# Kernel tuning notes

Hardware: AMD Instinct MI355X
Metric: run time of the kernel (lower is better)

Reference implementation:

```python
import jax, jax.numpy as jnp
import numpy as np

EPS = 1e-05
FACT = 2.0
REJECT_RATIO = 1.0


def setup_inputs() -> dict:
    key = jax.random.key(0)
    k1, k2 = jax.random.split(key)
    B, N = 8, 4096
    pc1 = jax.random.normal(k1, (B, 4, N), dtype=jnp.float32)
    pc2 = jax.random.normal(k2, (B, 4, N), dtype=jnp.float32)
    # homogeneous coordinates: last row = 1
    pc1 = pc1.at[:, 3, :].set(1.0)
    pc2 = pc2.at[:, 3, :].set(1.0)
    return {"pc1": pc1, "pc2": pc2}


def _rot_to_quat(R):
    # standard rotation-matrix -> quaternion (w, x, y, z)
    r00, r11, r22 = R[0, 0], R[1, 1], R[2, 2]
    qw = 0.5 * jnp.sqrt(jnp.maximum(1e-12, 1.0 + r00 + r11 + r22))
    qx = 0.5 * jnp.sqrt(jnp.maximum(0.0, 1.0 + r00 - r11 - r22))
    qy = 0.5 * jnp.sqrt(jnp.maximum(0.0, 1.0 - r00 + r11 - r22))
    qz = 0.5 * jnp.sqrt(jnp.maximum(0.0, 1.0 - r00 - r11 + r22))
    qx = jnp.where(R[2, 1] - R[1, 2] < 0, -qx, qx)
    qy = jnp.where(R[0, 2] - R[2, 0] < 0, -qy, qy)
    qz = jnp.where(R[1, 0] - R[0, 1] < 0, -qz, qz)
    return jnp.stack([qw, qx, qy, qz])


def _normalize_rotmat(R):
    # operates on COLUMNS, like the torch code (R[:, 2] etc.)
    z = R[:, 2] / jnp.linalg.norm(R[:, 2])
    y = R[:, 1]
    x = jnp.cross(y, z)
    x = x / jnp.linalg.norm(x)
    y = jnp.cross(z, x)
    return jnp.stack([x, y, z], axis=1)


def _norm_tf(pc):
    # T = diag(1/std) @ [I | -mean]  (std is unbiased, as torch.std)
    std = jnp.std(pc[:3, :], axis=1, ddof=1)
    mean = jnp.mean(pc[:3, :], axis=1)
    T = jnp.zeros((4, 4), dtype=pc.dtype)
    T = T.at[jnp.arange(3), jnp.arange(3)].set(1.0 / std)
    T = T.at[:3, 3].set(-mean / std)
    T = T.at[3, 3].set(1.0)
    return T


def _per_sample(pc1, pc2):
    # ---- soft_knn: pairwise squared distance over xyz ----
    p1, p2 = pc1[:3], pc2[:3]  # (3, N)
    d = ((p1 ** 2).sum(0)[:, None]
         - 2.0 * jnp.einsum('dn,dm->nm', p1, p2)
         + (p2 ** 2).sum(0)[None, :])            # (N1, N2)
    W = jax.nn.softmax(FACT / jnp.clip(d, EPS, None), axis=1)
    pc_nearest = pc2 @ W.T                        # (4, N1) soft-gathered points

    # ---- soft_outlier_rejection ----
    dist = jnp.linalg.norm(pc1 - pc_nearest, axis=0)
    filt = jax.nn.sigmoid((dist - dist.mean() * REJECT_RATIO - EPS) * -1e10)

    # ---- dlt(pc1, pc_nearest, filt) ----
    T2 = _norm_tf(pc_nearest)
    pc2n = T2 @ pc_nearest
    T1 = _norm_tf(pc1)
    pc1n = T1 @ pc1

    mask = (filt > 0.5).astype(pc1.dtype)         # hard inlier mask (sigmoid slope 1e10)
    N = pc1.shape[1]
    a = pc1n.T                                    # (N, 4)
    z4 = jnp.zeros((N, 4), dtype=pc1.dtype)
    row0 = jnp.concatenate([z4, -pc2n[2][:, None] * a, pc2n[1][:, None] * a], axis=1)
    row1 = jnp.concatenate([pc2n[2][:, None] * a, z4, -pc2n[0][:, None] * a], axis=1)
    M = (jnp.stack([row0, row1], axis=1) * mask[:, None, None]).reshape(2 * N, 12)

    _, _, Vh = jnp.linalg.svd(M, full_matrices=False)
    p = Vh[-1]                                    # null-space vector (12,)
    p = jnp.where(p[10] < 0, -p, p)
    p = p / jnp.sqrt(p[8] ** 2 + p[9] ** 2 + p[10] ** 2)

    T = jnp.zeros((4, 4), dtype=pc1.dtype)
    T = T.at[:3, :].set(p.reshape(3, 4)).at[3, 3].set(1.0)
    T = jnp.linalg.inv(T2) @ T @ T1
    R = _normalize_rotmat(T[:3, :3])
    T = T.at[:3, :3].set(R)
    return T, _rot_to_quat(R), T[:3, 3]


def reference(pc1, pc2):
    T, q, t = jax.vmap(_per_sample)(pc1, pc2)
    return T, q, t
```

## Files before the change

### kernel.cpp

```cpp
#include <hip/hip_runtime.h>
#include <math.h>

#define NPTS 4096
#define EPSC 1e-5f
#define F2C (2.0f*1.44269504088896340736f)

#if __has_builtin(__builtin_amdgcn_exp2f)
#define FEXP2 __builtin_amdgcn_exp2f
#else
#define FEXP2(x) __expf((x)*0.6931471805599453f)
#endif

#define IDX(i,j) ((i)*((i)+1)/2 + (j))

template<int CHN>
__global__ void __launch_bounds__(256) k_soft(const float* __restrict__ pc1,
                                              const float* __restrict__ pc2,
                                              float* __restrict__ part){
  constexpr int NC = NPTS/CHN;
  int bid = blockIdx.x;
  int chunk = bid & (NC-1), rb = (bid/NC) & 15, b = bid/(NC*16);

  __shared__ float4 sp[CHN];
  {
    const float* p2 = pc2 + (size_t)b*4*NPTS + chunk*CHN;
    for (int m = threadIdx.x; m < CHN; m += 256){
      float x = p2[m], y = p2[m+NPTS], z = p2[m+2*NPTS];
      sp[m] = make_float4(x, y, z, x*x + y*y + z*z);
    }
  }
  __syncthreads();

  int n = rb*256 + threadIdx.x;
  const float* p1 = pc1 + (size_t)b*4*NPTS + n;
  float x1 = p1[0], y1 = p1[NPTS], z1 = p1[2*NPTS];
  float q1 = x1*x1 + y1*y1 + z1*z1;
  float mx = -2.f*x1, my = -2.f*y1, mz = -2.f*z1;

  float4 c0 = sp[0];
  float d0 = fmaf(mx,c0.x, fmaf(my,c0.y, fmaf(mz,c0.z, c0.w + q1)));
  float m_ = F2C * __builtin_amdgcn_rcpf(fmaxf(d0, EPSC));
  float L = 1.f, Ax = c0.x, Ay = c0.y, Az = c0.z;

  #pragma unroll 8
  for (int mm=1; mm<CHN; ++mm){
    float4 c = sp[mm];
    float d = fmaf(mx,c.x, fmaf(my,c.y, fmaf(mz,c.z, c.w + q1)));
    float dinv = __builtin_amdgcn_rcpf(fmaxf(d, EPSC));
    float t = fmaf(F2C, dinv, -m_);
    if (__any(t > 0.f)){
      float tp = fmaxf(t, 0.f);
      float sc = FEXP2(-tp);
      L *= sc; Ax *= sc; Ay *= sc; Az *= sc;
      m_ += tp;
      t = fminf(t, 0.f);
    }
    float pe = FEXP2(t);
    L += pe;
    Ax = fmaf(pe,c.x,Ax); Ay = fmaf(pe,c.y,Ay); Az = fmaf(pe,c.z,Az);
  }
  float* pp = part + ((size_t)(b*NC + chunk)*5)*NPTS + n;
  pp[0]=m_; pp[NPTS]=L; pp[2*NPTS]=Ax; pp[3*NPTS]=Ay; pp[4*NPTS]=Az;
}

template<int NC>
__global__ void __launch_bounds__(512) k_merge(const float* __restrict__ pc1,
                                               const float* __restrict__ part,
                                               float* __restrict__ pcn,
                                               float* __restrict__ dist,
                                               float* __restrict__ psum13){
  int b = blockIdx.x >> 4, rb = blockIdx.x & 15;
  int t = threadIdx.x & 255, half = threadIdx.x >> 8;
  int n = rb*256 + t;
  constexpr int H = NC/2;
  float sc[H], Lc[H], Axc[H], Ayc[H], Azc[H];
  float S = -3.4e38f;
  #pragma unroll
  for (int c=0;c<H;c++){
    const float* pp = part + ((size_t)(b*NC + half*H + c)*5)*NPTS + n;
    sc[c]=pp[0]; Lc[c]=pp[NPTS]; Axc[c]=pp[2*NPTS]; Ayc[c]=pp[3*NPTS]; Azc[c]=pp[4*NPTS];
    S = fmaxf(S, sc[c]);
  }
  float L=0.f, Ax=0.f, Ay=0.f, Az=0.f;
  #pragma unroll
  for (int c=0;c<H;c++){
    float w = FEXP2(sc[c]-S);
    L=fmaf(w,Lc[c],L); Ax=fmaf(w,Axc[c],Ax); Ay=fmaf(w,Ayc[c],Ay); Az=fmaf(w,Azc[c],Az);
  }
  __shared__ float ex[256][5];
  if (half==1){ ex[t][0]=S; ex[t][1]=L; ex[t][2]=Ax; ex[t][3]=Ay; ex[t][4]=Az; }
  __syncthreads();
  __shared__ float red[4][13];
  if (half==0){
    float S1=ex[t][0];
    float M = fmaxf(S,S1);
    float w0=FEXP2(S-M), w1=FEXP2(S1-M);
    L = w0*L + w1*ex[t][1];
    Ax = w0*Ax + w1*ex[t][2];
    Ay = w0*Ay + w1*ex[t][3];
    Az = w0*Az + w1*ex[t][4];
    float inv = 1.f/L;
    float px=Ax*inv, py=Ay*inv, pz=Az*inv;
    const float* p1 = pc1 + (size_t)b*4*NPTS + n;
    float x1=p1[0], y1=p1[NPTS], z1=p1[2*NPTS];
    float dx=x1-px, dy=y1-py, dz=z1-pz;
    float dd=sqrtf(dx*dx+dy*dy+dz*dz);
    pcn[(size_t)(b*3+0)*NPTS+n]=px;
    pcn[(size_t)(b*3+1)*NPTS+n]=py;
    pcn[(size_t)(b*3+2)*NPTS+n]=pz;
    dist[(size_t)b*NPTS+n]=dd;
    float acc[13]={x1,y1,z1,x1*x1,y1*y1,z1*z1,px,py,pz,px*px,py*py,pz*pz,dd};
    int lane = t & 63, wv = t >> 6;
    #pragma unroll
    for (int k=0;k<13;k++){
      float v = acc[k];
      v += __shfl_xor(v,32); v += __shfl_xor(v,16); v += __shfl_xor(v,8);
      v += __shfl_xor(v,4);  v += __shfl_xor(v,2);  v += __shfl_xor(v,1);
      if (lane==0) red[wv][k]=v;
    }
  }
  __syncthreads();
  if (threadIdx.x<13)
    psum13[(size_t)blockIdx.x*13 + threadIdx.x] =
      red[0][threadIdx.x]+red[1][threadIdx.x]+red[2][threadIdx.x]+red[3][threadIdx.x];
}

__device__ __forceinline__ float elemA(const float* S, int i, int k){
  int bi=i>>2, bj=k>>2;
  int ii=i&3, jj=k&3;
  int lo = ii<jj?ii:jj, hi = ii<jj?jj:ii;
  int pe = 4*lo - ((lo*(lo-1))>>1) + (hi-lo);
  int w;
  if (bi==bj) w = (bi==2)?30:0;
  else {
    int blo = bi<bj?bi:bj, bhi = bi<bj?bj:bi;
    if (blo==0 && bhi==1) return 0.f;
    w = (blo==0)?10:20;
  }
  return S[w+pe];
}

__global__ void __launch_bounds__(256) k_solve(const float* __restrict__ pc1,
                                               const float* __restrict__ pcn,
                                               const float* __restrict__ dist,
                                               const float* __restrict__ psum13,
                                               float* __restrict__ out){
  int b=blockIdx.x, t=threadIdx.x;
  __shared__ float stot[13];
  __shared__ float sst[13];
  if (t<13){
    float s=0.f;
    #pragma unroll
    for (int i=0;i<16;i++) s += psum13[(size_t)(b*16+i)*13 + t];
    stot[t]=s;
  }
  __syncthreads();
  if (t==0){
    const float Nf = 4096.f, Nm1 = 4095.f;
    #pragma unroll
    for (int j=0;j<3;j++){
      float m  = stot[j]/Nf;
      float v  = (stot[3+j]-Nf*m*m)/Nm1;
      sst[j]=m; sst[3+j]=sqrtf(fmaxf(v,0.f));
      float m2 = stot[6+j]/Nf;
      float v2 = (stot[9+j]-Nf*m2*m2)/Nm1;
      sst[6+j]=m2; sst[9+j]=sqrtf(fmaxf(v2,0.f));
    }
    sst[12]=stot[12]/Nf;
  }
  __syncthreads();
  float i1x=1.f/sst[3], i1y=1.f/sst[4], i1z=1.f/sst[5];
  float t1x=-sst[0]/sst[3], t1y=-sst[1]/sst[4], t1z=-sst[2]/sst[5];
  float i2x=1.f/sst[9], i2y=1.f/sst[10], i2z=1.f/sst[11];
  float t2x=-sst[6]/sst[9], t2y=-sst[7]/sst[10], t2z=-sst[8]/sst[11];
  float meanD=sst[12];

  float acc[40];
  #pragma unroll
  for (int k=0;k<40;k++) acc[k]=0.f;
  #pragma unroll 4
  for (int i=0;i<16;i++){
    int n=i*256+t;
    const float* p1 = pc1 + (size_t)b*4*NPTS + n;
    float X1=fmaf(p1[0],i1x,t1x), Y1=fmaf(p1[NPTS],i1y,t1y), Z1=fmaf(p1[2*NPTS],i1z,t1z);
    float X2=fmaf(pcn[(size_t)(b*3+0)*NPTS+n],i2x,t2x);
    float Y2=fmaf(pcn[(size_t)(b*3+1)*NPTS+n],i2y,t2y);
    float Z2=fmaf(pcn[(size_t)(b*3+2)*NPTS+n],i2z,t2z);
    float zthr = (dist[(size_t)b*NPTS+n] - meanD) - EPSC;
    float msk = (zthr < 0.f) ? 1.f : 0.f;
    float tz = msk*Z2;
    float wA = tz*Z2, wB = -tz*X2, wC = -tz*Y2;
    float wD = msk*fmaf(X2,X2,Y2*Y2);
    float ee[10]={X1*X1, X1*Y1, X1*Z1, X1, Y1*Y1, Y1*Z1, Y1, Z1*Z1, Z1, 1.f};
    #pragma unroll
    for (int j=0;j<10;j++){
      acc[j]    = fmaf(wA,ee[j],acc[j]);
      acc[10+j] = fmaf(wB,ee[j],acc[10+j]);
      acc[20+j] = fmaf(wC,ee[j],acc[20+j]);
      acc[30+j] = fmaf(wD,ee[j],acc[30+j]);
    }
  }
  __shared__ float red[4][40];
  __shared__ float SS[40];
  {
    int lane=t&63, wv=t>>6;
    #pragma unroll
    for (int k=0;k<40;k++){
      float v=acc[k];
      v+=__shfl_xor(v,32); v+=__shfl_xor(v,16); v+=__shfl_xor(v,8);
      v+=__shfl_xor(v,4);  v+=__shfl_xor(v,2);  v+=__shfl_xor(v,1);
      if(lane==0) red[wv][k]=v;
    }
  }
  __syncthreads();
  if (t<40) SS[t]=red[0][t]+red[1][t]+red[2][t]+red[3][t];
  __syncthreads();

  if (t<64){
    float a[78];
    #pragma unroll
    for (int i=0;i<12;i++)
      #pragma unroll
      for (int j=0;j<=i;j++)
        a[IDX(i,j)] = elemA(SS,i,j);
    {
      float tr=0.f;
      #pragma unroll
      for (int i=0;i<12;i++) tr += a[IDX(i,i)];
      float eps = 1e-5f * tr * (1.f/12.f);
      #pragma unroll
      for (int i=0;i<12;i++) a[IDX(i,i)] += eps;
    }
    #pragma unroll
    for (int j=0;j<12;j++){
      float s = a[IDX(j,j)];
      #pragma unroll
      for (int k=0;k<j;k++) s = fmaf(-a[IDX(j,k)], a[IDX(j,k)], s);
      float d = sqrtf(fmaxf(s, 1e-30f));
      a[IDX(j,j)] = d;
      float dinv = __builtin_amdgcn_rcpf(d);
      #pragma unroll
      for (int i=j+1;i<12;i++){
        float s2 = a[IDX(i,j)];
        #pragma unroll
        for (int k=0;k<j;k++) s2 = fmaf(-a[IDX(i,k)], a[IDX(j,k)], s2);
        a[IDX(i,j)] = s2 * dinv;
      }
    }
    float y[12], Brow[12];
    #pragma unroll
    for (int i=0;i<12;i++){
      float s = (i==t) ? 1.f : 0.f;
      #pragma unroll
      for (int k=0;k<i;k++) s = fmaf(-a[IDX(i,k)], y[k], s);
      y[i] = s * __builtin_amdgcn_rcpf(a[IDX(i,i)]);
    }
    #pragma unroll
    for (int i=11;i>=0;i--){
      float s = y[i];
      #pragma unroll
      for (int k=11;k>i;k--) s = fmaf(-a[IDX(k,i)], Brow[k], s);
      Brow[i] = s * __builtin_amdgcn_rcpf(a[IDX(i,i)]);
    }
    {
      float mxv = 0.f;
      #pragma unroll
      for (int i=0;i<12;i++) mxv = fmaxf(mxv, fabsf(Brow[i]));
      mxv = fmaxf(mxv, __shfl_xor(mxv,1)); mxv = fmaxf(mxv, __shfl_xor(mxv,2));
      mxv = fmaxf(mxv, __shfl_xor(mxv,4)); mxv = fmaxf(mxv, __shfl_xor(mxv,8));
      float sc = __builtin_amdgcn_rcpf(mxv);
      #pragma unroll
      for (int i=0;i<12;i++) Brow[i] *= sc;
    }
    #pragma unroll
    for (int rep=0; rep<2; ++rep){
      float nr[12];
      #pragma unroll
      for (int i=0;i<12;i++) nr[i]=0.f;
      #pragma unroll
      for (int k=0;k<12;k++){
        float bjk = Brow[k];
        #pragma unroll
        for (int m2=0;m2<12;m2++){
          float bkm = __shfl(Brow[m2], k);
          nr[m2] = fmaf(bjk, bkm, nr[m2]);
        }
      }
      float mxv = 0.f;
      #pragma unroll
      for (int i=0;i<12;i++) mxv = fmaxf(mxv, fabsf(nr[i]));
      mxv = fmaxf(mxv, __shfl_xor(mxv,1)); mxv = fmaxf(mxv, __shfl_xor(mxv,2));
      mxv = fmaxf(mxv, __shfl_xor(mxv,4)); mxv = fmaxf(mxv, __shfl_xor(mxv,8));
      float sc = __builtin_amdgcn_rcpf(mxv);
      #pragma unroll
      for (int i=0;i<12;i++) Brow[i] = nr[i]*sc;
    }
    float v = 0.f;
    #pragma unroll
    for (int i=0;i<12;i++) v += Brow[i];
    #pragma unroll
    for (int it=0; it<14; ++it){
      float w = 0.f;
      #pragma unroll
      for (int k=0;k<12;k++) w = fmaf(Brow[k], __shfl(v,k), w);
      float nn = w*w;
      nn += __shfl_xor(nn,1); nn += __shfl_xor(nn,2);
      nn += __shfl_xor(nn,4); nn += __shfl_xor(nn,8);
      v = w * rsqrtf(nn);
    }
    float pvf[12];
    #pragma unroll
    for (int i=0;i<12;i++) pvf[i] = __shfl(v, i);

    if (t==0){
      double pv[12];
      #pragma unroll
      for (int i=0;i<12;i++) pv[i]=(double)pvf[i];
      if (pv[10]<0.0){
        #pragma unroll
        for (int i=0;i<12;i++) pv[i]=-pv[i];
      }
      double nrm = sqrt(pv[8]*pv[8]+pv[9]*pv[9]+pv[10]*pv[10]);
      #pragma unroll
      for (int i=0;i<12;i++) pv[i]/=nrm;
      double m1[3]={sst[0],sst[1],sst[2]}, sd1[3]={sst[3],sst[4],sst[5]};
      double m2[3]={sst[6],sst[7],sst[8]}, sd2[3]={sst[9],sst[10],sst[11]};
      double Td[3][4]={{pv[0],pv[1],pv[2],pv[3]},
                       {pv[4],pv[5],pv[6],pv[7]},
                       {pv[8],pv[9],pv[10],pv[11]}};
      double F[3][4];
      for (int i=0;i<3;i++){
        double b3 = Td[i][3];
        for (int j=0;j<3;j++){
          F[i][j] = sd2[i]*(Td[i][j]/sd1[j]);
          b3 += Td[i][j]*(-m1[j]/sd1[j]);
        }
        F[i][3] = sd2[i]*b3 + m2[i];
      }
      double zx=F[0][2],zy=F[1][2],zz2=F[2][2];
      double zn=sqrt(zx*zx+zy*zy+zz2*zz2);
      zx/=zn; zy/=zn; zz2/=zn;
      double yx=F[0][1],yy=F[1][1],yz=F[2][1];
      double xx=yy*zz2-yz*zy, xy=yz*zx-yx*zz2, xz=yx*zy-yy*zx;
      double xn=sqrt(xx*xx+xy*xy+xz*xz);
      xx/=xn; xy/=xn; xz/=xn;
      double y2x=zy*xz-zz2*xy, y2y=zz2*xx-zx*xz, y2z=zx*xy-zy*xx;
      double R00=xx,R01=y2x,R02=zx;
      double R10=xy,R11=y2y,R12=zy;
      double R20=xz,R21=y2z,R22=zz2;
      float* oT = out + b*16;
      oT[0]=(float)R00; oT[1]=(float)R01; oT[2]=(float)R02; oT[3]=(float)F[0][3];
      oT[4]=(float)R10; oT[5]=(float)R11; oT[6]=(float)R12; oT[7]=(float)F[1][3];
      oT[8]=(float)R20; oT[9]=(float)R21; oT[10]=(float)R22; oT[11]=(float)F[2][3];
      oT[12]=0.f; oT[13]=0.f; oT[14]=0.f; oT[15]=1.f;
      double qw=0.5*sqrt(fmax(1e-12, 1.0+R00+R11+R22));
      double qx=0.5*sqrt(fmax(0.0, 1.0+R00-R11-R22));
      double qy=0.5*sqrt(fmax(0.0, 1.0-R00+R11-R22));
      double qz=0.5*sqrt(fmax(0.0, 1.0-R00-R11+R22));
      if (R21-R12<0.0) qx=-qx;
      if (R02-R20<0.0) qy=-qy;
      if (R10-R01<0.0) qz=-qz;
      float* oQ = out + 128 + b*4;
      oQ[0]=(float)qw; oQ[1]=(float)qx; oQ[2]=(float)qy; oQ[3]=(float)qz;
      float* ot3 = out + 160 + b*3;
      ot3[0]=(float)F[0][3]; ot3[1]=(float)F[1][3]; ot3[2]=(float)F[2][3];
    }
  }
}

extern "C" void kernel_launch(void* const* d_in, const int* in_sizes, int n_in,
                              void* d_out, int out_size, void* d_ws, size_t ws_size,
                              hipStream_t stream) {
  const float* pc1 = (const float*)d_in[0];
  const float* pc2 = (const float*)d_in[1];
  float* out  = (float*)d_out;
  float* ws   = (float*)d_ws;

  const size_t fixed = 98304 + 32768 + 128*13;
  size_t need16 = ((size_t)8*16*5*NPTS + fixed) * 4;
  int NC = (ws_size >= need16) ? 16 : 8;

  float* part  = ws;
  float* pcn   = part + (size_t)8*NC*5*NPTS;
  float* dist  = pcn + 98304;
  float* psum13= dist + 32768;

  if (NC == 16){
    hipLaunchKernelGGL(k_soft<256>,  dim3(2048), dim3(256), 0, stream, pc1, pc2, part);
    hipLaunchKernelGGL(k_merge<16>,  dim3(128),  dim3(512), 0, stream, pc1, part, pcn, dist, psum13);
  } else {
    hipLaunchKernelGGL(k_soft<512>,  dim3(1024), dim3(256), 0, stream, pc1, pc2, part);
    hipLaunchKernelGGL(k_merge<8>,   dim3(128),  dim3(512), 0, stream, pc1, part, pcn, dist, psum13);
  }
  hipLaunchKernelGGL(k_solve, dim3(8), dim3(256), 0, stream, pc1, pcn, dist, psum13, out);
}
```

Baseline: 156.9 us.

## Skip negligible softmax terms via min-distance prepass and split solve kernel

The soft-kNN kernel now does a first pass to find the minimum distance per query, fixing the softmax max up front. In a second pass it skips whole groups of four candidates when every lane's weight would be below exp2(-100), which removes the online rescaling and most of the exp and reciprocal work. The 40-term moment accumulation moves out of the single-block-per-batch solve into a separate 64-block kernel, leaving a small finalize kernel for the solve. The chunk count is fixed at 8 rather than chosen from workspace size. The cost is an extra distance pass, one more kernel launch, and dropping terms that are numerically negligible.

```diff
diff --git a/kernel.cpp b/kernel.cpp
--- a/kernel.cpp
+++ b/kernel.cpp
@@ -4,6 +4,7 @@
 #define NPTS 4096
 #define EPSC 1e-5f
 #define F2C (2.0f*1.44269504088896340736f)
+#define SKIP_MARGIN 100.0f
 
 #if __has_builtin(__builtin_amdgcn_exp2f)
 #define FEXP2 __builtin_amdgcn_exp2f
@@ -37,27 +38,34 @@
   float q1 = x1*x1 + y1*y1 + z1*z1;
   float mx = -2.f*x1, my = -2.f*y1, mz = -2.f*z1;
 
-  float4 c0 = sp[0];
-  float d0 = fmaf(mx,c0.x, fmaf(my,c0.y, fmaf(mz,c0.z, c0.w + q1)));
-  float m_ = F2C * __builtin_amdgcn_rcpf(fmaxf(d0, EPSC));
-  float L = 1.f, Ax = c0.x, Ay = c0.y, Az = c0.z;
-
+  float dmin = 3.4e38f;
   #pragma unroll 8
-  for (int mm=1; mm<CHN; ++mm){
-    float4 c = sp[mm];
+  for (int m=0; m<CHN; ++m){
+    float4 c = sp[m];
     float d = fmaf(mx,c.x, fmaf(my,c.y, fmaf(mz,c.z, c.w + q1)));
-    float dinv = __builtin_amdgcn_rcpf(fmaxf(d, EPSC));
-    float t = fmaf(F2C, dinv, -m_);
-    if (__any(t > 0.f)){
-      float tp = fmaxf(t, 0.f);
-      float sc = FEXP2(-tp);
-      L *= sc; Ax *= sc; Ay *= sc; Az *= sc;
-      m_ += tp;
-      t = fminf(t, 0.f);
-    }
-    float pe = FEXP2(t);
-    L += pe;
-    Ax = fmaf(pe,c.x,Ax); Ay = fmaf(pe,c.y,Ay); Az = fmaf(pe,c.z,Az);
+    dmin = fminf(dmin, d);
+  }
+  float m_ = F2C * __builtin_amdgcn_rcpf(fmaxf(dmin, EPSC));
+  float r  = m_ - SKIP_MARGIN;
+  float d_thr = (r > 0.f) ? F2C * __builtin_amdgcn_rcpf(r) : 3.4e38f;
+
+  float L=0.f, Ax=0.f, Ay=0.f, Az=0.f;
+  for (int g=0; g<CHN; g+=4){
+    float4 c0=sp[g], c1=sp[g+1], c2=sp[g+2], c3=sp[g+3];
+    float d0 = fmaf(mx,c0.x, fmaf(my,c0.y, fmaf(mz,c0.z, c0.w + q1)));
+    float d1 = fmaf(mx,c1.x, fmaf(my,c1.y, fmaf(mz,c1.z, c1.w + q1)));
+    float d2 = fmaf(mx,c2.x, fmaf(my,c2.y, fmaf(mz,c2.z, c2.w + q1)));
+    float d3 = fmaf(mx,c3.x, fmaf(my,c3.y, fmaf(mz,c3.z, c3.w + q1)));
+    float gmin = fminf(fminf(d0,d1), fminf(d2,d3));
+    if (__all(gmin > d_thr)) continue;
+    float p0 = FEXP2(fmaf(F2C, __builtin_amdgcn_rcpf(fmaxf(d0,EPSC)), -m_));
+    float p1e= FEXP2(fmaf(F2C, __builtin_amdgcn_rcpf(fmaxf(d1,EPSC)), -m_));
+    float p2e= FEXP2(fmaf(F2C, __builtin_amdgcn_rcpf(fmaxf(d2,EPSC)), -m_));
+    float p3e= FEXP2(fmaf(F2C, __builtin_amdgcn_rcpf(fmaxf(d3,EPSC)), -m_));
+    L += (p0+p1e)+(p2e+p3e);
+    Ax = fmaf(p0,c0.x, fmaf(p1e,c1.x, fmaf(p2e,c2.x, fmaf(p3e,c3.x, Ax))));
+    Ay = fmaf(p0,c0.y, fmaf(p1e,c1.y, fmaf(p2e,c2.y, fmaf(p3e,c3.y, Ay))));
+    Az = fmaf(p0,c0.z, fmaf(p1e,c1.z, fmaf(p2e,c2.z, fmaf(p3e,c3.z, Az))));
   }
   float* pp = part + ((size_t)(b*NC + chunk)*5)*NPTS + n;
   pp[0]=m_; pp[NPTS]=L; pp[2*NPTS]=Ax; pp[3*NPTS]=Ay; pp[4*NPTS]=Az;
@@ -125,6 +133,83 @@
       red[0][threadIdx.x]+red[1][threadIdx.x]+red[2][threadIdx.x]+red[3][threadIdx.x];
 }
 
+__device__ __forceinline__ void stats_from_tot(const float* stot, float* sst){
+  const float Nf = 4096.f, Nm1 = 4095.f;
+  #pragma unroll
+  for (int j=0;j<3;j++){
+    float m  = stot[j]/Nf;
+    float v  = (stot[3+j]-Nf*m*m)/Nm1;
+    sst[j]=m; sst[3+j]=sqrtf(fmaxf(v,0.f));
+    float m2 = stot[6+j]/Nf;
+    float v2 = (stot[9+j]-Nf*m2*m2)/Nm1;
+    sst[6+j]=m2; sst[9+j]=sqrtf(fmaxf(v2,0.f));
+  }
+  sst[12]=stot[12]/Nf;
+}
+
+__global__ void __launch_bounds__(256) k_acc(const float* __restrict__ pc1,
+                                             const float* __restrict__ pcn,
+                                             const float* __restrict__ dist,
+                                             const float* __restrict__ psum13,
+                                             float* __restrict__ psum40){
+  int b = blockIdx.x >> 3, sl = blockIdx.x & 7, t = threadIdx.x;
+  __shared__ float stot[13];
+  __shared__ float sst[13];
+  if (t<13){
+    float s=0.f;
+    #pragma unroll
+    for (int i=0;i<16;i++) s += psum13[(size_t)(b*16+i)*13 + t];
+    stot[t]=s;
+  }
+  __syncthreads();
+  if (t==0) stats_from_tot(stot, sst);
+  __syncthreads();
+  float i1x=1.f/sst[3], i1y=1.f/sst[4], i1z=1.f/sst[5];
+  float t1x=-sst[0]/sst[3], t1y=-sst[1]/sst[4], t1z=-sst[2]/sst[5];
+  float i2x=1.f/sst[9], i2y=1.f/sst[10], i2z=1.f/sst[11];
+  float t2x=-sst[6]/sst[9], t2y=-sst[7]/sst[10], t2z=-sst[8]/sst[11];
+  float meanD=sst[12];
+
+  float acc[40];
+  #pragma unroll
+  for (int k=0;k<40;k++) acc[k]=0.f;
+  #pragma unroll
+  for (int i=0;i<2;i++){
+    int n = sl*512 + i*256 + t;
+    const float* p1 = pc1 + (size_t)b*4*NPTS + n;
+    float X1=fmaf(p1[0],i1x,t1x), Y1=fmaf(p1[NPTS],i1y,t1y), Z1=fmaf(p1[2*NPTS],i1z,t1z);
+    float X2=fmaf(pcn[(size_t)(b*3+0)*NPTS+n],i2x,t2x);
+    float Y2=fmaf(pcn[(size_t)(b*3+1)*NPTS+n],i2y,t2y);
+    float Z2=fmaf(pcn[(size_t)(b*3+2)*NPTS+n],i2z,t2z);
+    float zthr = (dist[(size_t)b*NPTS+n] - meanD) - EPSC;
+    float msk = (zthr < 0.f) ? 1.f : 0.f;
+    float tz = msk*Z2;
+    float wA = tz*Z2, wB = -tz*X2, wC = -tz*Y2;
+    float wD = msk*fmaf(X2,X2,Y2*Y2);
+    float ee[10]={X1*X1, X1*Y1, X1*Z1, X1, Y1*Y1, Y1*Z1, Y1, Z1*Z1, Z1, 1.f};
+    #pragma unroll
+    for (int j=0;j<10;j++){
+      acc[j]    = fmaf(wA,ee[j],acc[j]);
+      acc[10+j] = fmaf(wB,ee[j],acc[10+j]);
+      acc[20+j] = fmaf(wC,ee[j],acc[20+j]);
+      acc[30+j] = fmaf(wD,ee[j],acc[30+j]);
+    }
+  }
+  __shared__ float red[4][40];
+  {
+    int lane=t&63, wv=t>>6;
+    #pragma unroll
+    for (int k=0;k<40;k++){
+      float v=acc[k];
+      v+=__shfl_xor(v,32); v+=__shfl_xor(v,16); v+=__shfl_xor(v,8);
+      v+=__shfl_xor(v,4);  v+=__shfl_xor(v,2);  v+=__shfl_xor(v,1);
+      if(lane==0) red[wv][k]=v;
+    }
+  }
+  __syncthreads();
+  if (t<40) psum40[(size_t)blockIdx.x*40 + t] = red[0][t]+red[1][t]+red[2][t]+red[3][t];
+}
+
 __device__ __forceinline__ float elemA(const float* S, int i, int k){
   int bi=i>>2, bj=k>>2;
   int ii=i&3, jj=k&3;
@@ -140,14 +225,19 @@
   return S[w+pe];
 }
 
-__global__ void __launch_bounds__(256) k_solve(const float* __restrict__ pc1,
-                                               const float* __restrict__ pcn,
-                                               const float* __restrict__ dist,
-                                               const float* __restrict__ psum13,
-                                               float* __restrict__ out){
+__global__ void __launch_bounds__(64) k_fin(const float* __restrict__ psum13,
+                                            const float* __restrict__ psum40,
+                                            float* __restrict__ out){
   int b=blockIdx.x, t=threadIdx.x;
+  __shared__ float SS[40];
   __shared__ float stot[13];
   __shared__ float sst[13];
+  if (t<40){
+    float s=0.f;
+    #pragma unroll
+    for (int i=0;i<8;i++) s += psum40[(size_t)(b*8+i)*40 + t];
+    SS[t]=s;
+  }
   if (t<13){
     float s=0.f;
     #pragma unroll
@@ -155,216 +245,156 @@
     stot[t]=s;
   }
   __syncthreads();
+  if (t==0) stats_from_tot(stot, sst);
+  __syncthreads();
+
+  float a[78];
+  #pragma unroll
+  for (int i=0;i<12;i++)
+    #pragma unroll
+    for (int j=0;j<=i;j++)
+      a[IDX(i,j)] = elemA(SS,i,j);
+  {
+    float tr=0.f;
+    #pragma unroll
+    for (int i=0;i<12;i++) tr += a[IDX(i,i)];
+    float eps = 1e-5f * tr * (1.f/12.f);
+    #pragma unroll
+    for (int i=0;i<12;i++) a[IDX(i,i)] += eps;
+  }
+  #pragma unroll
+  for (int j=0;j<12;j++){
+    float s = a[IDX(j,j)];
+    #pragma unroll
+    for (int k=0;k<j;k++) s = fmaf(-a[IDX(j,k)], a[IDX(j,k)], s);
+    float d = sqrtf(fmaxf(s, 1e-30f));
+    a[IDX(j,j)] = d;
+    float dinv = __builtin_amdgcn_rcpf(d);
+    #pragma unroll
+    for (int i=j+1;i<12;i++){
+      float s2 = a[IDX(i,j)];
+      #pragma unroll
+      for (int k=0;k<j;k++) s2 = fmaf(-a[IDX(i,k)], a[IDX(j,k)], s2);
+      a[IDX(i,j)] = s2 * dinv;
+    }
+  }
+  float y[12], Brow[12];
+  #pragma unroll
+  for (int i=0;i<12;i++){
+    float s = (i==t) ? 1.f : 0.f;
+    #pragma unroll
+    for (int k=0;k<i;k++) s = fmaf(-a[IDX(i,k)], y[k], s);
+    y[i] = s * __builtin_amdgcn_rcpf(a[IDX(i,i)]);
+  }
+  #pragma unroll
+  for (int i=11;i>=0;i--){
+    float s = y[i];
+    #pragma unroll
+    for (int k=11;k>i;k--) s = fmaf(-a[IDX(k,i)], Brow[k], s);
+    Brow[i] = s * __builtin_amdgcn_rcpf(a[IDX(i,i)]);
+  }
+  {
+    float mxv = 0.f;
+    #pragma unroll
+    for (int i=0;i<12;i++) mxv = fmaxf(mxv, fabsf(Brow[i]));
+    mxv = fmaxf(mxv, __shfl_xor(mxv,1)); mxv = fmaxf(mxv, __shfl_xor(mxv,2));
+    mxv = fmaxf(mxv, __shfl_xor(mxv,4)); mxv = fmaxf(mxv, __shfl_xor(mxv,8));
+    float sc = __builtin_amdgcn_rcpf(mxv);
+    #pragma unroll
+    for (int i=0;i<12;i++) Brow[i] *= sc;
+  }
+  #pragma unroll
+  for (int rep=0; rep<2; ++rep){
+    float nr[12];
+    #pragma unroll
+    for (int i=0;i<12;i++) nr[i]=0.f;
+    #pragma unroll
+    for (int k=0;k<12;k++){
+      float bjk = Brow[k];
+      #pragma unroll
+      for (int m2=0;m2<12;m2++){
+        float bkm = __shfl(Brow[m2], k);
+        nr[m2] = fmaf(bjk, bkm, nr[m2]);
+      }
+    }
+    float mxv = 0.f;
+    #pragma unroll
+    for (int i=0;i<12;i++) mxv = fmaxf(mxv, fabsf(nr[i]));
+    mxv = fmaxf(mxv, __shfl_xor(mxv,1)); mxv = fmaxf(mxv, __shfl_xor(mxv,2));
+    mxv = fmaxf(mxv, __shfl_xor(mxv,4)); mxv = fmaxf(mxv, __shfl_xor(mxv,8));
+    float sc = __builtin_amdgcn_rcpf(mxv);
+    #pragma unroll
+    for (int i=0;i<12;i++) Brow[i] = nr[i]*sc;
+  }
+  float v = 0.f;
+  #pragma unroll
+  for (int i=0;i<12;i++) v += Brow[i];
+  #pragma unroll
+  for (int it=0; it<14; ++it){
+    float w = 0.f;
+    #pragma unroll
+    for (int k=0;k<12;k++) w = fmaf(Brow[k], __shfl(v,k), w);
+    float nn = w*w;
+    nn += __shfl_xor(nn,1); nn += __shfl_xor(nn,2);
+    nn += __shfl_xor(nn,4); nn += __shfl_xor(nn,8);
+    v = w * rsqrtf(nn);
+  }
+  float pvf[12];
+  #pragma unroll
+  for (int i=0;i<12;i++) pvf[i] = __shfl(v, i);
+
   if (t==0){
-    const float Nf = 4096.f, Nm1 = 4095.f;
-    #pragma unroll
-    for (int j=0;j<3;j++){
-      float m  = stot[j]/Nf;
-      float v  = (stot[3+j]-Nf*m*m)/Nm1;
-      sst[j]=m; sst[3+j]=sqrtf(fmaxf(v,0.f));
-      float m2 = stot[6+j]/Nf;
-      float v2 = (stot[9+j]-Nf*m2*m2)/Nm1;
-      sst[6+j]=m2; sst[9+j]=sqrtf(fmaxf(v2,0.f));
-    }
-    sst[12]=stot[12]/Nf;
-  }
-  __syncthreads();
-  float i1x=1.f/sst[3], i1y=1.f/sst[4], i1z=1.f/sst[5];
-  float t1x=-sst[0]/sst[3], t1y=-sst[1]/sst[4], t1z=-sst[2]/sst[5];
-  float i2x=1.f/sst[9], i2y=1.f/sst[10], i2z=1.f/sst[11];
-  float t2x=-sst[6]/sst[9], t2y=-sst[7]/sst[10], t2z=-sst[8]/sst[11];
-  float meanD=sst[12];
-
-  float acc[40];
-  #pragma unroll
-  for (int k=0;k<40;k++) acc[k]=0.f;
-  #pragma unroll 4
-  for (int i=0;i<16;i++){
-    int n=i*256+t;
-    const float* p1 = pc1 + (size_t)b*4*NPTS + n;
-    float X1=fmaf(p1[0],i1x,t1x), Y1=fmaf(p1[NPTS],i1y,t1y), Z1=fmaf(p1[2*NPTS],i1z,t1z);
-    float X2=fmaf(pcn[(size_t)(b*3+0)*NPTS+n],i2x,t2x);
-    float Y2=fmaf(pcn[(size_t)(b*3+1)*NPTS+n],i2y,t2y);
-    float Z2=fmaf(pcn[(size_t)(b*3+2)*NPTS+n],i2z,t2z);
-    float zthr = (dist[(size_t)b*NPTS+n] - meanD) - EPSC;
-    float msk = (zthr < 0.f) ? 1.f : 0.f;
-    float tz = msk*Z2;
-    float wA = tz*Z2, wB = -tz*X2, wC = -tz*Y2;
-    float wD = msk*fmaf(X2,X2,Y2*Y2);
-    float ee[10]={X1*X1, X1*Y1, X1*Z1, X1, Y1*Y1, Y1*Z1, Y1, Z1*Z1, Z1, 1.f};
-    #pragma unroll
-    for (int j=0;j<10;j++){
-      acc[j]    = fmaf(wA,ee[j],acc[j]);
-      acc[10+j] = fmaf(wB,ee[j],acc[10+j]);
-      acc[20+j] = fmaf(wC,ee[j],acc[20+j]);
-      acc[30+j] = fmaf(wD,ee[j],acc[30+j]);
-    }
-  }
-  __shared__ float red[4][40];
-  __shared__ float SS[40];
-  {
-    int lane=t&63, wv=t>>6;
-    #pragma unroll
-    for (int k=0;k<40;k++){
-      float v=acc[k];
-      v+=__shfl_xor(v,32); v+=__shfl_xor(v,16); v+=__shfl_xor(v,8);
-      v+=__shfl_xor(v,4);  v+=__shfl_xor(v,2);  v+=__shfl_xor(v,1);
-      if(lane==0) red[wv][k]=v;
-    }
-  }
-  __syncthreads();
-  if (t<40) SS[t]=red[0][t]+red[1][t]+red[2][t]+red[3][t];
-  __syncthreads();
-
-  if (t<64){
-    float a[78];
-    #pragma unroll
-    for (int i=0;i<12;i++)
+    double pv[12];
+    #pragma unroll
+    for (int i=0;i<12;i++) pv[i]=(double)pvf[i];
+    if (pv[10]<0.0){
       #pragma unroll
-      for (int j=0;j<=i;j++)
-        a[IDX(i,j)] = elemA(SS,i,j);
-    {
-      float tr=0.f;
-      #pragma unroll
-      for (int i=0;i<12;i++) tr += a[IDX(i,i)];
-      float eps = 1e-5f * tr * (1.f/12.f);
-      #pragma unroll
-      for (int i=0;i<12;i++) a[IDX(i,i)] += eps;
-    }
-    #pragma unroll
-    for (int j=0;j<12;j++){
-      float s = a[IDX(j,j)];
-      #pragma unroll
-      for (int k=0;k<j;k++) s = fmaf(-a[IDX(j,k)], a[IDX(j,k)], s);
-      float d = sqrtf(fmaxf(s, 1e-30f));
-      a[IDX(j,j)] = d;
-      float dinv = __builtin_amdgcn_rcpf(d);
-      #pragma unroll
-      for (int i=j+1;i<12;i++){
-        float s2 = a[IDX(i,j)];
-        #pragma unroll
-        for (int k=0;k<j;k++) s2 = fmaf(-a[IDX(i,k)], a[IDX(j,k)], s2);
-        a[IDX(i,j)] = s2 * dinv;
+      for (int i=0;i<12;i++) pv[i]=-pv[i];
+    }
+    double nrm = sqrt(pv[8]*pv[8]+pv[9]*pv[9]+pv[10]*pv[10]);
+    #pragma unroll
+    for (int i=0;i<12;i++) pv[i]/=nrm;
+    double m1[3]={sst[0],sst[1],sst[2]}, sd1[3]={sst[3],sst[4],sst[5]};
+    double m2[3]={sst[6],sst[7],sst[8]}, sd2[3]={sst[9],sst[10],sst[11]};
+    double Td[3][4]={{pv[0],pv[1],pv[2],pv[3]},
+                     {pv[4],pv[5],pv[6],pv[7]},
+                     {pv[8],pv[9],pv[10],pv[11]}};
+    double F[3][4];
+    for (int i=0;i<3;i++){
+      double b3 = Td[i][3];
+      for (int j=0;j<3;j++){
+        F[i][j] = sd2[i]*(Td[i][j]/sd1[j]);
+        b3 += Td[i][j]*(-m1[j]/sd1[j]);
       }
-    }
-    float y[12], Brow[12];
-    #pragma unroll
-    for (int i=0;i<12;i++){
-      float s = (i==t) ? 1.f : 0.f;
-      #pragma unroll
-      for (int k=0;k<i;k++) s = fmaf(-a[IDX(i,k)], y[k], s);
-      y[i] = s * __builtin_amdgcn_rcpf(a[IDX(i,i)]);
-    }
-    #pragma unroll
-    for (int i=11;i>=0;i--){
-      float s = y[i];
-      #pragma unroll
-      for (int k=11;k>i;k--) s = fmaf(-a[IDX(k,i)], Brow[k], s);
-      Brow[i] = s * __builtin_amdgcn_rcpf(a[IDX(i,i)]);
-    }
-    {
-      float mxv = 0.f;
-      #pragma unroll
-      for (int i=0;i<12;i++) mxv = fmaxf(mxv, fabsf(Brow[i]));
-      mxv = fmaxf(mxv, __shfl_xor(mxv,1)); mxv = fmaxf(mxv, __shfl_xor(mxv,2));
-      mxv = fmaxf(mxv, __shfl_xor(mxv,4)); mxv = fmaxf(mxv, __shfl_xor(mxv,8));
-      float sc = __builtin_amdgcn_rcpf(mxv);
-      #pragma unroll
-      for (int i=0;i<12;i++) Brow[i] *= sc;
-    }
-    #pragma unroll
-    for (int rep=0; rep<2; ++rep){
-      float nr[12];
-      #pragma unroll
-      for (int i=0;i<12;i++) nr[i]=0.f;
-      #pragma unroll
-      for (int k=0;k<12;k++){
-        float bjk = Brow[k];
-        #pragma unroll
-        for (int m2=0;m2<12;m2++){
-          float bkm = __shfl(Brow[m2], k);
-          nr[m2] = fmaf(bjk, bkm, nr[m2]);
-        }
-      }
-      float mxv = 0.f;
-      #pragma unroll
-      for (int i=0;i<12;i++) mxv = fmaxf(mxv, fabsf(nr[i]));
-      mxv = fmaxf(mxv, __shfl_xor(mxv,1)); mxv = fmaxf(mxv, __shfl_xor(mxv,2));
-      mxv = fmaxf(mxv, __shfl_xor(mxv,4)); mxv = fmaxf(mxv, __shfl_xor(mxv,8));
-      float sc = __builtin_amdgcn_rcpf(mxv);
-      #pragma unroll
-      for (int i=0;i<12;i++) Brow[i] = nr[i]*sc;
-    }
-    float v = 0.f;
-    #pragma unroll
-    for (int i=0;i<12;i++) v += Brow[i];
-    #pragma unroll
-    for (int it=0; it<14; ++it){
-      float w = 0.f;
-      #pragma unroll
-      for (int k=0;k<12;k++) w = fmaf(Brow[k], __shfl(v,k), w);
-      float nn = w*w;
-      nn += __shfl_xor(nn,1); nn += __shfl_xor(nn,2);
-      nn += __shfl_xor(nn,4); nn += __shfl_xor(nn,8);
-      v = w * rsqrtf(nn);
-    }
-    float pvf[12];
-    #pragma unroll
-    for (int i=0;i<12;i++) pvf[i] = __shfl(v, i);
-
-    if (t==0){
-      double pv[12];
-      #pragma unroll
-      for (int i=0;i<12;i++) pv[i]=(double)pvf[i];
-      if (pv[10]<0.0){
-        #pragma unroll
-        for (int i=0;i<12;i++) pv[i]=-pv[i];
-      }
-      double nrm = sqrt(pv[8]*pv[8]+pv[9]*pv[9]+pv[10]*pv[10]);
-      #pragma unroll
-      for (int i=0;i<12;i++) pv[i]/=nrm;
-      double m1[3]={sst[0],sst[1],sst[2]}, sd1[3]={sst[3],sst[4],sst[5]};
-      double m2[3]={sst[6],sst[7],sst[8]}, sd2[3]={sst[9],sst[10],sst[11]};
-      double Td[3][4]={{pv[0],pv[1],pv[2],pv[3]},
-                       {pv[4],pv[5],pv[6],pv[7]},
-                       {pv[8],pv[9],pv[10],pv[11]}};
-      double F[3][4];
-      for (int i=0;i<3;i++){
-        double b3 = Td[i][3];
-        for (int j=0;j<3;j++){
-          F[i][j] = sd2[i]*(Td[i][j]/sd1[j]);
-          b3 += Td[i][j]*(-m1[j]/sd1[j]);
-        }
-        F[i][3] = sd2[i]*b3 + m2[i];
-      }
-      double zx=F[0][2],zy=F[1][2],zz2=F[2][2];
-      double zn=sqrt(zx*zx+zy*zy+zz2*zz2);
-      zx/=zn; zy/=zn; zz2/=zn;
-      double yx=F[0][1],yy=F[1][1],yz=F[2][1];
-      double xx=yy*zz2-yz*zy, xy=yz*zx-yx*zz2, xz=yx*zy-yy*zx;
-      double xn=sqrt(xx*xx+xy*xy+xz*xz);
-      xx/=xn; xy/=xn; xz/=xn;
-      double y2x=zy*xz-zz2*xy, y2y=zz2*xx-zx*xz, y2z=zx*xy-zy*xx;
-      double R00=xx,R01=y2x,R02=zx;
-      double R10=xy,R11=y2y,R12=zy;
-      double R20=xz,R21=y2z,R22=zz2;
-      float* oT = out + b*16;
-      oT[0]=(float)R00; oT[1]=(float)R01; oT[2]=(float)R02; oT[3]=(float)F[0][3];
-      oT[4]=(float)R10; oT[5]=(float)R11; oT[6]=(float)R12; oT[7]=(float)F[1][3];
-      oT[8]=(float)R20; oT[9]=(float)R21; oT[10]=(float)R22; oT[11]=(float)F[2][3];
-      oT[12]=0.f; oT[13]=0.f; oT[14]=0.f; oT[15]=1.f;
-      double qw=0.5*sqrt(fmax(1e-12, 1.0+R00+R11+R22));
-      double qx=0.5*sqrt(fmax(0.0, 1.0+R00-R11-R22));
-      double qy=0.5*sqrt(fmax(0.0, 1.0-R00+R11-R22));
-      double qz=0.5*sqrt(fmax(0.0, 1.0-R00-R11+R22));
-      if (R21-R12<0.0) qx=-qx;
-      if (R02-R20<0.0) qy=-qy;
-      if (R10-R01<0.0) qz=-qz;
-      float* oQ = out + 128 + b*4;
-      oQ[0]=(float)qw; oQ[1]=(float)qx; oQ[2]=(float)qy; oQ[3]=(float)qz;
-      float* ot3 = out + 160 + b*3;
-      ot3[0]=(float)F[0][3]; ot3[1]=(float)F[1][3]; ot3[2]=(float)F[2][3];
-    }
+      F[i][3] = sd2[i]*b3 + m2[i];
+    }
+    double zx=F[0][2],zy=F[1][2],zz2=F[2][2];
+    double zn=sqrt(zx*zx+zy*zy+zz2*zz2);
+    zx/=zn; zy/=zn; zz2/=zn;
+    double yx=F[0][1],yy=F[1][1],yz=F[2][1];
+    double xx=yy*zz2-yz*zy, xy=yz*zx-yx*zz2, xz=yx*zy-yy*zx;
+    double xn=sqrt(xx*xx+xy*xy+xz*xz);
+    xx/=xn; xy/=xn; xz/=xn;
+    double y2x=zy*xz-zz2*xy, y2y=zz2*xx-zx*xz, y2z=zx*xy-zy*xx;
+    double R00=xx,R01=y2x,R02=zx;
+    double R10=xy,R11=y2y,R12=zy;
+    double R20=xz,R21=y2z,R22=zz2;
+    float* oT = out + b*16;
+    oT[0]=(float)R00; oT[1]=(float)R01; oT[2]=(float)R02; oT[3]=(float)F[0][3];
+    oT[4]=(float)R10; oT[5]=(float)R11; oT[6]=(float)R12; oT[7]=(float)F[1][3];
+    oT[8]=(float)R20; oT[9]=(float)R21; oT[10]=(float)R22; oT[11]=(float)F[2][3];
+    oT[12]=0.f; oT[13]=0.f; oT[14]=0.f; oT[15]=1.f;
+    double qw=0.5*sqrt(fmax(1e-12, 1.0+R00+R11+R22));
+    double qx=0.5*sqrt(fmax(0.0, 1.0+R00-R11-R22));
+    double qy=0.5*sqrt(fmax(0.0, 1.0-R00+R11-R22));
+    double qz=0.5*sqrt(fmax(0.0, 1.0-R00-R11+R22));
+    if (R21-R12<0.0) qx=-qx;
+    if (R02-R20<0.0) qy=-qy;
+    if (R10-R01<0.0) qz=-qz;
+    float* oQ = out + 128 + b*4;
+    oQ[0]=(float)qw; oQ[1]=(float)qx; oQ[2]=(float)qy; oQ[3]=(float)qz;
+    float* ot3 = out + 160 + b*3;
+    ot3[0]=(float)F[0][3]; ot3[1]=(float)F[1][3]; ot3[2]=(float)F[2][3];
   }
 }
 
@@ -376,21 +406,14 @@
   float* out  = (float*)d_out;
   float* ws   = (float*)d_ws;
 
-  const size_t fixed = 98304 + 32768 + 128*13;
-  size_t need16 = ((size_t)8*16*5*NPTS + fixed) * 4;
-  int NC = (ws_size >= need16) ? 16 : 8;
-
   float* part  = ws;
-  float* pcn   = part + (size_t)8*NC*5*NPTS;
+  float* pcn   = part + 1310720;
   float* dist  = pcn + 98304;
   float* psum13= dist + 32768;
-
-  if (NC == 16){
-    hipLaunchKernelGGL(k_soft<256>,  dim3(2048), dim3(256), 0, stream, pc1, pc2, part);
-    hipLaunchKernelGGL(k_merge<16>,  dim3(128),  dim3(512), 0, stream, pc1, part, pcn, dist, psum13);
-  } else {
-    hipLaunchKernelGGL(k_soft<512>,  dim3(1024), dim3(256), 0, stream, pc1, pc2, part);
-    hipLaunchKernelGGL(k_merge<8>,   dim3(128),  dim3(512), 0, stream, pc1, part, pcn, dist, psum13);
-  }
-  hipLaunchKernelGGL(k_solve, dim3(8), dim3(256), 0, stream, pc1, pcn, dist, psum13, out);
-}
+  float* psum40= psum13 + 1664;
+
+  hipLaunchKernelGGL(k_soft<512>, dim3(1024), dim3(256), 0, stream, pc1, pc2, part);
+  hipLaunchKernelGGL(k_merge<8>,  dim3(128),  dim3(512), 0, stream, pc1, part, pcn, dist, psum13);
+  hipLaunchKernelGGL(k_acc,       dim3(64),   dim3(256), 0, stream, pc1, pcn, dist, psum13, psum40);
+  hipLaunchKernelGGL(k_fin,       dim3(8),    dim3(64),  0, stream, psum13, psum40, out);
+}
```

Result: slower. 195.1 us (+24.4%).

## Fuse partial-softmax merge into the solve kernel and pack partials as float4

Applied to the files above, without the earlier changes.

Removes the separate merge kernel. Each of the 8 per-batch solve blocks now merges the 16 chunk partials itself, keeps the soft-nearest points and distances in LDS instead of global memory, and computes the normalization statistics in-block. Partials are stored as a float4 plus a separate z array, so each element takes two vector loads instead of five scalar loads. This saves one launch and the pcn/dist/psum global round trip. In exchange, only 8 blocks now read the full partial buffer, which reduces parallelism for that phase, and the fallback for a small workspace has been dropped.

```diff
diff --git a/kernel.cpp b/kernel.cpp
--- a/kernel.cpp
+++ b/kernel.cpp
@@ -13,11 +13,11 @@
 
 #define IDX(i,j) ((i)*((i)+1)/2 + (j))
 
-template<int CHN>
 __global__ void __launch_bounds__(256) k_soft(const float* __restrict__ pc1,
                                               const float* __restrict__ pc2,
-                                              float* __restrict__ part){
-  constexpr int NC = NPTS/CHN;
+                                              float4* __restrict__ part4,
+                                              float* __restrict__ partZ){
+  constexpr int CHN = 256, NC = 16;
   int bid = blockIdx.x;
   int chunk = bid & (NC-1), rb = (bid/NC) & 15, b = bid/(NC*16);
 
@@ -59,70 +59,23 @@
     L += pe;
     Ax = fmaf(pe,c.x,Ax); Ay = fmaf(pe,c.y,Ay); Az = fmaf(pe,c.z,Az);
   }
-  float* pp = part + ((size_t)(b*NC + chunk)*5)*NPTS + n;
-  pp[0]=m_; pp[NPTS]=L; pp[2*NPTS]=Ax; pp[3*NPTS]=Ay; pp[4*NPTS]=Az;
-}
-
-template<int NC>
-__global__ void __launch_bounds__(512) k_merge(const float* __restrict__ pc1,
-                                               const float* __restrict__ part,
-                                               float* __restrict__ pcn,
-                                               float* __restrict__ dist,
-                                               float* __restrict__ psum13){
-  int b = blockIdx.x >> 4, rb = blockIdx.x & 15;
-  int t = threadIdx.x & 255, half = threadIdx.x >> 8;
-  int n = rb*256 + t;
-  constexpr int H = NC/2;
-  float sc[H], Lc[H], Axc[H], Ayc[H], Azc[H];
-  float S = -3.4e38f;
-  #pragma unroll
-  for (int c=0;c<H;c++){
-    const float* pp = part + ((size_t)(b*NC + half*H + c)*5)*NPTS + n;
-    sc[c]=pp[0]; Lc[c]=pp[NPTS]; Axc[c]=pp[2*NPTS]; Ayc[c]=pp[3*NPTS]; Azc[c]=pp[4*NPTS];
-    S = fmaxf(S, sc[c]);
-  }
-  float L=0.f, Ax=0.f, Ay=0.f, Az=0.f;
-  #pragma unroll
-  for (int c=0;c<H;c++){
-    float w = FEXP2(sc[c]-S);
-    L=fmaf(w,Lc[c],L); Ax=fmaf(w,Axc[c],Ax); Ay=fmaf(w,Ayc[c],Ay); Az=fmaf(w,Azc[c],Az);
-  }
-  __shared__ float ex[256][5];
-  if (half==1){ ex[t][0]=S; ex[t][1]=L; ex[t][2]=Ax; ex[t][3]=Ay; ex[t][4]=Az; }
-  __syncthreads();
-  __shared__ float red[4][13];
-  if (half==0){
-    float S1=ex[t][0];
-    float M = fmaxf(S,S1);
-    float w0=FEXP2(S-M), w1=FEXP2(S1-M);
-    L = w0*L + w1*ex[t][1];
-    Ax = w0*Ax + w1*ex[t][2];
-    Ay = w0*Ay + w1*ex[t][3];
-    Az = w0*Az + w1*ex[t][4];
-    float inv = 1.f/L;
-    float px=Ax*inv, py=Ay*inv, pz=Az*inv;
-    const float* p1 = pc1 + (size_t)b*4*NPTS + n;
-    float x1=p1[0], y1=p1[NPTS], z1=p1[2*NPTS];
-    float dx=x1-px, dy=y1-py, dz=z1-pz;
-    float dd=sqrtf(dx*dx+dy*dy+dz*dz);
-    pcn[(size_t)(b*3+0)*NPTS+n]=px;
-    pcn[(size_t)(b*3+1)*NPTS+n]=py;
-    pcn[(size_t)(b*3+2)*NPTS+n]=pz;
-    dist[(size_t)b*NPTS+n]=dd;
-    float acc[13]={x1,y1,z1,x1*x1,y1*y1,z1*z1,px,py,pz,px*px,py*py,pz*pz,dd};
-    int lane = t & 63, wv = t >> 6;
-    #pragma unroll
-    for (int k=0;k<13;k++){
-      float v = acc[k];
-      v += __shfl_xor(v,32); v += __shfl_xor(v,16); v += __shfl_xor(v,8);
-      v += __shfl_xor(v,4);  v += __shfl_xor(v,2);  v += __shfl_xor(v,1);
-      if (lane==0) red[wv][k]=v;
-    }
-  }
-  __syncthreads();
-  if (threadIdx.x<13)
-    psum13[(size_t)blockIdx.x*13 + threadIdx.x] =
-      red[0][threadIdx.x]+red[1][threadIdx.x]+red[2][threadIdx.x]+red[3][threadIdx.x];
+  size_t idx = (size_t)(b*NC + chunk)*NPTS + n;
+  part4[idx] = make_float4(m_, L, Ax, Ay);
+  partZ[idx] = Az;
+}
+
+__device__ __forceinline__ void stats_from_tot(const float* stot, float* sst){
+  const float Nf = 4096.f, Nm1 = 4095.f;
+  #pragma unroll
+  for (int j=0;j<3;j++){
+    float m  = stot[j]/Nf;
+    float v  = (stot[3+j]-Nf*m*m)/Nm1;
+    sst[j]=m; sst[3+j]=sqrtf(fmaxf(v,0.f));
+    float m2 = stot[6+j]/Nf;
+    float v2 = (stot[9+j]-Nf*m2*m2)/Nm1;
+    sst[6+j]=m2; sst[9+j]=sqrtf(fmaxf(v2,0.f));
+  }
+  sst[12]=stot[12]/Nf;
 }
 
 __device__ __forceinline__ float elemA(const float* S, int i, int k){
@@ -140,35 +93,76 @@
   return S[w+pe];
 }
 
-__global__ void __launch_bounds__(256) k_solve(const float* __restrict__ pc1,
-                                               const float* __restrict__ pcn,
-                                               const float* __restrict__ dist,
-                                               const float* __restrict__ psum13,
-                                               float* __restrict__ out){
-  int b=blockIdx.x, t=threadIdx.x;
+__global__ void __launch_bounds__(512) k_tail(const float* __restrict__ pc1,
+                                              const float4* __restrict__ part4,
+                                              const float* __restrict__ partZ,
+                                              float* __restrict__ out){
+  constexpr int NC = 16;
+  int b = blockIdx.x, t = threadIdx.x;
+  int lane = t & 63, wv = t >> 6;
+
+  __shared__ float4 rowdat[NPTS];
+  __shared__ float red13[8][13];
+  __shared__ float red40[8][40];
   __shared__ float stot[13];
   __shared__ float sst[13];
+  __shared__ float SS[40];
+
+  float acc13[13];
+  #pragma unroll
+  for (int k=0;k<13;k++) acc13[k]=0.f;
+  for (int i=0;i<8;i++){
+    int n = i*512 + t;
+    float4 f[NC]; float zz[NC];
+    #pragma unroll
+    for (int c=0;c<NC;c++){
+      size_t idx = (size_t)(b*NC + c)*NPTS + n;
+      f[c]  = part4[idx];
+      zz[c] = partZ[idx];
+    }
+    float S = f[0].x;
+    #pragma unroll
+    for (int c=1;c<NC;c++) S = fmaxf(S, f[c].x);
+    float L=0.f, Ax=0.f, Ay=0.f, Az=0.f;
+    #pragma unroll
+    for (int c=0;c<NC;c++){
+      float w = FEXP2(f[c].x - S);
+      L  = fmaf(w, f[c].y, L);
+      Ax = fmaf(w, f[c].z, Ax);
+      Ay = fmaf(w, f[c].w, Ay);
+      Az = fmaf(w, zz[c],  Az);
+    }
+    float inv = 1.f/L;
+    float px=Ax*inv, py=Ay*inv, pz=Az*inv;
+    const float* p1 = pc1 + (size_t)b*4*NPTS + n;
+    float x1=p1[0], y1=p1[NPTS], z1=p1[2*NPTS];
+    float dx=x1-px, dy=y1-py, dz=z1-pz;
+    float dd=sqrtf(dx*dx+dy*dy+dz*dz);
+    rowdat[n] = make_float4(px,py,pz,dd);
+    acc13[0]+=x1;    acc13[1]+=y1;    acc13[2]+=z1;
+    acc13[3]+=x1*x1; acc13[4]+=y1*y1; acc13[5]+=z1*z1;
+    acc13[6]+=px;    acc13[7]+=py;    acc13[8]+=pz;
+    acc13[9]+=px*px; acc13[10]+=py*py; acc13[11]+=pz*pz;
+    acc13[12]+=dd;
+  }
+  #pragma unroll
+  for (int k=0;k<13;k++){
+    float v = acc13[k];
+    v += __shfl_xor(v,32); v += __shfl_xor(v,16); v += __shfl_xor(v,8);
+    v += __shfl_xor(v,4);  v += __shfl_xor(v,2);  v += __shfl_xor(v,1);
+    if (lane==0) red13[wv][k]=v;
+  }
+  __syncthreads();
   if (t<13){
     float s=0.f;
     #pragma unroll
-    for (int i=0;i<16;i++) s += psum13[(size_t)(b*16+i)*13 + t];
+    for (int w=0;w<8;w++) s += red13[w][t];
     stot[t]=s;
   }
   __syncthreads();
-  if (t==0){
-    const float Nf = 4096.f, Nm1 = 4095.f;
-    #pragma unroll
-    for (int j=0;j<3;j++){
-      float m  = stot[j]/Nf;
-      float v  = (stot[3+j]-Nf*m*m)/Nm1;
-      sst[j]=m; sst[3+j]=sqrtf(fmaxf(v,0.f));
-      float m2 = stot[6+j]/Nf;
-      float v2 = (stot[9+j]-Nf*m2*m2)/Nm1;
-      sst[6+j]=m2; sst[9+j]=sqrtf(fmaxf(v2,0.f));
-    }
-    sst[12]=stot[12]/Nf;
-  }
-  __syncthreads();
+  if (t==0) stats_from_tot(stot, sst);
+  __syncthreads();
+
   float i1x=1.f/sst[3], i1y=1.f/sst[4], i1z=1.f/sst[5];
   float t1x=-sst[0]/sst[3], t1y=-sst[1]/sst[4], t1z=-sst[2]/sst[5];
   float i2x=1.f/sst[9], i2y=1.f/sst[10], i2z=1.f/sst[11];
@@ -178,15 +172,15 @@
   float acc[40];
   #pragma unroll
   for (int k=0;k<40;k++) acc[k]=0.f;
-  #pragma unroll 4
-  for (int i=0;i<16;i++){
-    int n=i*256+t;
+  for (int i=0;i<8;i++){
+    int n = i*512 + t;
     const float* p1 = pc1 + (size_t)b*4*NPTS + n;
     float X1=fmaf(p1[0],i1x,t1x), Y1=fmaf(p1[NPTS],i1y,t1y), Z1=fmaf(p1[2*NPTS],i1z,t1z);
-    float X2=fmaf(pcn[(size_t)(b*3+0)*NPTS+n],i2x,t2x);
-    float Y2=fmaf(pcn[(size_t)(b*3+1)*NPTS+n],i2y,t2y);
-    float Z2=fmaf(pcn[(size_t)(b*3+2)*NPTS+n],i2z,t2z);
-    float zthr = (dist[(size_t)b*NPTS+n] - meanD) - EPSC;
+    float4 rd = rowdat[n];
+    float X2=fmaf(rd.x,i2x,t2x);
+    float Y2=fmaf(rd.y,i2y,t2y);
+    float Z2=fmaf(rd.z,i2z,t2z);
+    float zthr = (rd.w - meanD) - EPSC;
     float msk = (zthr < 0.f) ? 1.f : 0.f;
     float tz = msk*Z2;
     float wA = tz*Z2, wB = -tz*X2, wC = -tz*Y2;
@@ -200,20 +194,20 @@
       acc[30+j] = fmaf(wD,ee[j],acc[30+j]);
     }
   }
-  __shared__ float red[4][40];
-  __shared__ float SS[40];
-  {
-    int lane=t&63, wv=t>>6;
-    #pragma unroll
-    for (int k=0;k<40;k++){
-      float v=acc[k];
-      v+=__shfl_xor(v,32); v+=__shfl_xor(v,16); v+=__shfl_xor(v,8);
-      v+=__shfl_xor(v,4);  v+=__shfl_xor(v,2);  v+=__shfl_xor(v,1);
-      if(lane==0) red[wv][k]=v;
-    }
-  }
-  __syncthreads();
-  if (t<40) SS[t]=red[0][t]+red[1][t]+red[2][t]+red[3][t];
+  #pragma unroll
+  for (int k=0;k<40;k++){
+    float v=acc[k];
+    v+=__shfl_xor(v,32); v+=__shfl_xor(v,16); v+=__shfl_xor(v,8);
+    v+=__shfl_xor(v,4);  v+=__shfl_xor(v,2);  v+=__shfl_xor(v,1);
+    if(lane==0) red40[wv][k]=v;
+  }
+  __syncthreads();
+  if (t<40){
+    float s=0.f;
+    #pragma unroll
+    for (int w=0;w<8;w++) s += red40[w][t];
+    SS[t]=s;
+  }
   __syncthreads();
 
   if (t<64){
@@ -376,21 +370,10 @@
   float* out  = (float*)d_out;
   float* ws   = (float*)d_ws;
 
-  const size_t fixed = 98304 + 32768 + 128*13;
-  size_t need16 = ((size_t)8*16*5*NPTS + fixed) * 4;
-  int NC = (ws_size >= need16) ? 16 : 8;
-
-  float* part  = ws;
-  float* pcn   = part + (size_t)8*NC*5*NPTS;
-  float* dist  = pcn + 98304;
-  float* psum13= dist + 32768;
-
-  if (NC == 16){
-    hipLaunchKernelGGL(k_soft<256>,  dim3(2048), dim3(256), 0, stream, pc1, pc2, part);
-    hipLaunchKernelGGL(k_merge<16>,  dim3(128),  dim3(512), 0, stream, pc1, part, pcn, dist, psum13);
-  } else {
-    hipLaunchKernelGGL(k_soft<512>,  dim3(1024), dim3(256), 0, stream, pc1, pc2, part);
-    hipLaunchKernelGGL(k_merge<8>,   dim3(128),  dim3(512), 0, stream, pc1, part, pcn, dist, psum13);
-  }
-  hipLaunchKernelGGL(k_solve, dim3(8), dim3(256), 0, stream, pc1, pcn, dist, psum13, out);
-}
+  float4* part4 = (float4*)ws;
+  float*  partZ = ws + 4*2097152/4 + 0;
+  partZ = ws + 2097152;
+
+  hipLaunchKernelGGL(k_soft, dim3(2048), dim3(256), 0, stream, pc1, pc2, part4, partZ);
+  hipLaunchKernelGGL(k_tail, dim3(8),    dim3(512), 0, stream, pc1, part4, partZ, out);
+}
```

Result: slower. 170.7 us (+8.8%).
